# Performance work log

Hardware: AMD Instinct MI355X
Metric: run time of the kernel (lower is better)

Reference implementation:

```python
import jax, jax.numpy as jnp
import numpy as np

D_IN = 1024
D_MODEL = 1024
NUM_HEADS = 16
DEPTH = D_MODEL // NUM_HEADS


def setup_inputs() -> dict:
    key = jax.random.key(0)
    ks = jax.random.split(key, 7)
    B, N = 2, 2048
    s = 1.0 / np.sqrt(D_IN)
    return {
        "x": jax.random.normal(ks[0], (B, N, D_IN), dtype=jnp.float32),
        "Wq": jax.random.normal(ks[1], (D_IN, D_MODEL), dtype=jnp.float32) * s,
        "bq": jnp.zeros((D_MODEL,), dtype=jnp.float32),
        "Wk": jax.random.normal(ks[2], (D_IN, D_MODEL), dtype=jnp.float32) * s,
        "bk": jnp.zeros((D_MODEL,), dtype=jnp.float32),
        "Wv": jax.random.normal(ks[3], (D_IN, D_MODEL), dtype=jnp.float32) * s,
        "bv": jnp.zeros((D_MODEL,), dtype=jnp.float32),
    }


def _split_heads(t):
    B, N, _ = t.shape
    return t.reshape(B, N, NUM_HEADS, DEPTH).transpose(0, 2, 1, 3)  # [B,H,N,depth]


def reference(x, Wq, bq, Wk, bk, Wv, bv):
    B, N, _ = x.shape
    q = _split_heads(x @ Wq + bq)
    k = _split_heads(x @ Wk + bk)
    v = _split_heads(x @ Wv + bv)
    scale = 1.0 / jnp.sqrt(jnp.float32(DEPTH))
    attn = jnp.einsum("bhnd,bhmd->bhnm", q, k) * scale  # [B,H,N,N]
    attn = jax.nn.softmax(attn, axis=-1)
    out = jnp.einsum("bhnm,bhmd->bhnd", attn, v)
    return out.transpose(0, 2, 1, 3).reshape(B, N, D_MODEL)
```

## Files before the change

kernel.cpp:

```cpp
#include <hip/hip_runtime.h>
#include <cstdint>


#define SEQ_N 2048
#define NHEAD 16
#define DEPTH 64
#define SCALE_Q (0.125f * 1.44269504088896340736f)
#define M_OFF (-12.0f)

typedef short bf16x8 __attribute__((ext_vector_type(8)));
typedef short short4v __attribute__((ext_vector_type(4)));
typedef float f32x4 __attribute__((ext_vector_type(4)));

#define MFMA32(a, b, c) __builtin_amdgcn_mfma_f32_16x16x32_bf16((a), (b), (c), 0, 0, 0)

#if defined(__has_builtin)
#if __has_builtin(__builtin_amdgcn_exp2f)
#define FEXP2(x) __builtin_amdgcn_exp2f(x)
#endif
#endif
#ifndef FEXP2
#define FEXP2(x) exp2f(x)
#endif

__device__ __forceinline__ short f2b(float f) {
    union { float f; unsigned u; } v; v.f = f;
    unsigned u = v.u;
    return (short)((u + 0x7FFFu + ((u >> 16) & 1u)) >> 16);
}

__device__ __forceinline__ unsigned cvt_pk_bf16(float lo, float hi) {
    unsigned r;
    asm("v_cvt_pk_bf16_f32 %0, %1, %2" : "=v"(r) : "v"(lo), "v"(hi));
    return r;
}

__device__ __forceinline__ void gld_lds16(const void* g, void* l) {
    __builtin_amdgcn_global_load_lds(
        (const __attribute__((address_space(1))) unsigned int*)(uintptr_t)g,
        (__attribute__((address_space(3))) unsigned int*)(uintptr_t)l, 16, 0, 0);
}

__global__ __launch_bounds__(256) void cvt_all_kernel(
    const float* __restrict__ x, short* __restrict__ xb,
    const float* __restrict__ Wq, const float* __restrict__ Wk,
    const float* __restrict__ Wv, short* __restrict__ WT)
{
    __shared__ float tile[64][65];
    if (blockIdx.x < 2048) {
        const int i = blockIdx.x * 256 + threadIdx.x;
        const float4* xi = (const float4*)x + (size_t)i * 2;
        const float4 a = xi[0], c = xi[1];
        bf16x8 o;
        o[0] = f2b(a.x); o[1] = f2b(a.y); o[2] = f2b(a.z); o[3] = f2b(a.w);
        o[4] = f2b(c.x); o[5] = f2b(c.y); o[6] = f2b(c.z); o[7] = f2b(c.w);
        *((bf16x8*)xb + i) = o;
        return;
    }
    const int bid = blockIdx.x - 2048;
    const int mat = bid >> 8;
    const int t = bid & 255;
    const int k0 = (t >> 4) * 64, n0 = (t & 15) * 64;
    const float* W = (mat == 0) ? Wq : ((mat == 1) ? Wk : Wv);
    const int tt = threadIdx.x;
#pragma unroll
    for (int i = 0; i < 16; ++i) {
        const int idx = tt + i * 256;
        const int r = idx >> 6, c = idx & 63;
        tile[r][c] = W[(size_t)(k0 + r) * 1024 + n0 + c];
    }
    __syncthreads();
#pragma unroll
    for (int i = 0; i < 16; ++i) {
        const int idx = tt + i * 256;
        const int r = idx >> 6, c = idx & 63;
        WT[(size_t)(mat * 1024 + n0 + r) * 1024 + k0 + c] = f2b(tile[c][r]);
    }
}

__global__ __launch_bounds__(512, 2) void qkv_gemm_kernel(
    const short* __restrict__ A, const short* __restrict__ BT,
    const float* __restrict__ bq, const float* __restrict__ bk, const float* __restrict__ bv,
    short* __restrict__ Qb, short* __restrict__ Kb, short* __restrict__ VTb)
{
    __shared__ __align__(16) short sm[57344];
    const int tid = threadIdx.x;
    const int l = tid & 63, w = tid >> 6;
    const int lr = l & 15, lk = l >> 4;
    const int wr = w >> 2, wcn = w & 3;

    const int id2 = (blockIdx.x & 7) * 32 + (blockIdx.x >> 3);
    const int bm = id2 & 15, bn = id2 >> 4;
    const int row0 = bm * 256, col0 = bn * 192;

    const int gsrc8 = ((tid & 7) ^ ((tid >> 3) & 7)) << 3;
    const short* a_src = A + (size_t)(row0 + (tid >> 3)) * 1024 + gsrc8;
    const short* b_src = BT + (size_t)(col0 + (tid >> 3)) * 1024 + gsrc8;

    const int aBase = (wr * 128 + lr) * 64;
    const int bBase = (wcn * 48 + lr) * 64;
    const int asw0 = ((lk)     ^ (lr & 7)) << 3;
    const int asw1 = ((lk + 4) ^ (lr & 7)) << 3;

    f32x4 acc[8][3];
#pragma unroll
    for (int m = 0; m < 8; ++m)
#pragma unroll
        for (int n = 0; n < 3; ++n) acc[m][n] = (f32x4){0.f, 0.f, 0.f, 0.f};

#define GSTAGE(BUF, KT)                                                    \
    do {                                                                   \
        short* asb = sm + (BUF) * 16384;                                   \
        short* bsb = sm + 32768 + (BUF) * 12288;                           \
        gld_lds16(a_src + (KT) * 64,          &asb[tid * 8]);              \
        gld_lds16(a_src + (KT) * 64 + 65536,  &asb[tid * 8 + 4096]);       \
        gld_lds16(a_src + (KT) * 64 + 131072, &asb[tid * 8 + 8192]);       \
        gld_lds16(a_src + (KT) * 64 + 196608, &asb[tid * 8 + 12288]);      \
        gld_lds16(b_src + (KT) * 64,          &bsb[tid * 8]);              \
        gld_lds16(b_src + (KT) * 64 + 65536,  &bsb[tid * 8 + 4096]);       \
        gld_lds16(b_src + (KT) * 64 + 131072, &bsb[tid * 8 + 8192]);       \
    } while (0)

    GSTAGE(0, 0);

#pragma unroll 2
    for (int kt = 0; kt < 16; ++kt) {
        const int cur = kt & 1;
        if (kt + 1 < 16) {
            GSTAGE(cur ^ 1, kt + 1);
            asm volatile("s_waitcnt vmcnt(7)" ::: "memory");
        } else {
            asm volatile("s_waitcnt vmcnt(0)" ::: "memory");
        }
        __builtin_amdgcn_s_barrier();
        __builtin_amdgcn_sched_barrier(0);

        const short* Al = sm + cur * 16384;
        const short* Bl = sm + 32768 + cur * 12288;

        bf16x8 bfv[3][2];
#pragma unroll
        for (int n = 0; n < 3; ++n) {
            bfv[n][0] = *(const bf16x8*)(Bl + bBase + n * 1024 + asw0);
            bfv[n][1] = *(const bf16x8*)(Bl + bBase + n * 1024 + asw1);
        }
#pragma unroll
        for (int m = 0; m < 8; ++m) {
            bf16x8 a0 = *(const bf16x8*)(Al + aBase + m * 1024 + asw0);
            bf16x8 a1 = *(const bf16x8*)(Al + aBase + m * 1024 + asw1);
#pragma unroll
            for (int n = 0; n < 3; ++n) {
                acc[m][n] = MFMA32(a0, bfv[n][0], acc[m][n]);
                acc[m][n] = MFMA32(a1, bfv[n][1], acc[m][n]);
            }
        }

        __builtin_amdgcn_sched_barrier(0);
        __builtin_amdgcn_s_barrier();
    }
#undef GSTAGE

    short* Cl = sm;
#pragma unroll
    for (int n = 0; n < 3; ++n) {
        const int gb = col0 + wcn * 48 + n * 16;
        const int mat = gb >> 10;
        const int jj = (gb + lr) & 1023;
        if (mat < 2) {
            const float bias = ((mat == 0) ? bq : bk)[jj];
            const float sc = (mat == 0) ? SCALE_Q : 1.0f;
            const int cc = wcn * 48 + n * 16 + lr;
#pragma unroll
            for (int m = 0; m < 8; ++m) {
                const int rbase = wr * 128 + m * 16 + lk * 4;
#pragma unroll
                for (int r = 0; r < 4; ++r)
                    Cl[(rbase + r) * 200 + cc] = f2b((acc[m][n][r] + bias) * sc);
            }
        } else {
            const float bias = bv[jj];
            const int h = jj >> 6, d = jj & 63;
#pragma unroll
            for (int m = 0; m < 8; ++m) {
                const int grow0 = row0 + wr * 128 + m * 16 + lk * 4;
                const int bb = grow0 >> 11, ns0 = grow0 & 2047;
                const int g = (ns0 >> 2) & 15;
                const int gp = (g & 8) | ((g & 3) << 1) | ((g >> 2) & 1);
                const int nsp = (ns0 & ~63) | (gp << 2);
                short4v pv;
#pragma unroll
                for (int r = 0; r < 4; ++r) pv[r] = f2b(acc[m][n][r] + bias);
                *(short4v*)(VTb + ((size_t)(bb * NHEAD + h) * DEPTH + d) * SEQ_N + nsp) = pv;
            }
        }
    }
    __syncthreads();
    {
        const int row = tid >> 1, half = tid & 1;
        const int grow = row0 + row;
        const int bb = grow >> 11, ns = grow & 2047;
#pragma unroll
        for (int i = 0; i < 12; ++i) {
            const int cc = half * 96 + i * 8;
            const int gc = col0 + cc;
            const int mat = gc >> 10;
            if (mat < 2) {
                short* O = mat ? Kb : Qb;
                const int h = (gc & 1023) >> 6, d0 = gc & 63;
                *(bf16x8*)(O + ((size_t)(bb * NHEAD + h) * SEQ_N + ns) * DEPTH + d0) =
                    *(const bf16x8*)(Cl + row * 200 + cc);
            }
        }
    }
}


__device__ __forceinline__ float exppack32_lane(const f32x4 s[4], bf16x8 pb[2]) {
    float rs = 0.f;
#pragma unroll
    for (int kk = 0; kk < 2; ++kk) {
        union { unsigned u[4]; bf16x8 v; } pk;
#pragma unroll
        for (int hh = 0; hh < 2; ++hh) {
            const int c = 2 * kk + hh;
            const float p0 = FEXP2(s[c][0]);
            const float p1 = FEXP2(s[c][1]);
            const float p2 = FEXP2(s[c][2]);
            const float p3 = FEXP2(s[c][3]);
            rs += (p0 + p1) + (p2 + p3);
            pk.u[2 * hh]     = cvt_pk_bf16(p0, p1);
            pk.u[2 * hh + 1] = cvt_pk_bf16(p2, p3);
        }
        pb[kk] = pk.v;
    }
    return rs;
}

#define NT 16

__global__ __launch_bounds__(256, 2) void attn_kernel(
    const short* __restrict__ Qb, const short* __restrict__ Kb,
    const short* __restrict__ VTb, float* __restrict__ out)
{
    __shared__ short smem[2][16384];

    const int tid = threadIdx.x;
    const int l = tid & 63, w = tid >> 6;
    const int lr = l & 15, lk = l >> 4;

    const int hb = blockIdx.x;
    const int slot = hb >> 3;
    const int bh = (hb & 7) * 4 + (slot >> 4);
    const int qt = slot & 15;
    const int b = bh >> 4, h = bh & 15;

    const int qw = qt * 128 + w * 32;

    const short* Qg = Qb + ((size_t)bh * SEQ_N + qw + lr) * DEPTH + lk * 8;
    const bf16x8 bq00 = *(const bf16x8*)(Qg);
    const bf16x8 bq01 = *(const bf16x8*)(Qg + 32);
    const bf16x8 bq10 = *(const bf16x8*)(Qg + 16 * DEPTH);
    const bf16x8 bq11 = *(const bf16x8*)(Qg + 16 * DEPTH + 32);

    const short* Kg = Kb + (size_t)bh * SEQ_N * DEPTH;
    const short* Vg = VTb + (size_t)bh * DEPTH * SEQ_N;

    const int srow = tid >> 3;
    const int sg = (tid & 7) ^ (srow & 7);
    const short* Ksrc = Kg + (size_t)srow * DEPTH + sg * 8;
    const short* Vsrc = Vg + (size_t)srow * SEQ_N + sg * 8;

#define STAGE(BUF, T)                                                            \
    do {                                                                         \
        const int key0_ = (T) * 128;                                             \
        short* dst = &smem[BUF][w * 512];                                        \
        gld_lds16(Ksrc + (size_t)key0_ * DEPTH, dst);                            \
        gld_lds16(Ksrc + (size_t)(key0_ + 32) * DEPTH, dst + 2048);              \
        gld_lds16(Ksrc + (size_t)(key0_ + 64) * DEPTH, dst + 4096);              \
        gld_lds16(Ksrc + (size_t)(key0_ + 96) * DEPTH, dst + 6144);              \
        gld_lds16(Vsrc + key0_, dst + 8192);                                     \
        gld_lds16(Vsrc + key0_ + 32 * SEQ_N, dst + 10240);                       \
        gld_lds16(Vsrc + key0_ + 64, dst + 12288);                               \
        gld_lds16(Vsrc + key0_ + 64 + 32 * SEQ_N, dst + 14336);                  \
    } while (0)

    const short* s0p = &smem[0][0];
    const int aoff0 = lr * 64 + (((lk    ) ^ (lr & 7)) << 3);
    const int aoff1 = lr * 64 + (((lk + 4) ^ (lr & 7)) << 3);

    f32x4 acc0[4], acc1[4];
#pragma unroll
    for (int n = 0; n < 4; ++n) {
        acc0[n] = (f32x4){0.f, 0.f, 0.f, 0.f};
        acc1[n] = (f32x4){0.f, 0.f, 0.f, 0.f};
    }
    float l0 = 0.f, l1 = 0.f;

    STAGE(0, 0);
    asm volatile("s_waitcnt vmcnt(0)" ::: "memory");
    __builtin_amdgcn_s_barrier();
    __builtin_amdgcn_sched_barrier(0);

#pragma unroll 2
    for (int t = 0; t < NT; ++t) {
        const int cur = t & 1;
        const int tn = (t + 1 < NT) ? (t + 1) : (NT - 1);
        STAGE(cur ^ 1, tn);

#pragma unroll
        for (int ss = 0; ss < 2; ++ss) {
            const int sub = ss ^ (w & 1);
            const short* Kl = s0p + cur * 16384 + sub * 4096;
            const short* Vl = Kl + 8192;

            bf16x8 kf[4][2], vf[4][2];
#pragma unroll
            for (int c = 0; c < 4; ++c) {
                kf[c][0] = *(const bf16x8*)(Kl + c * 1024 + aoff0);
                kf[c][1] = *(const bf16x8*)(Kl + c * 1024 + aoff1);
            }
#pragma unroll
            for (int n = 0; n < 4; ++n) {
                vf[n][0] = *(const bf16x8*)(Vl + n * 1024 + aoff0);
                vf[n][1] = *(const bf16x8*)(Vl + n * 1024 + aoff1);
            }

            f32x4 s0[4], s1[4];
            __builtin_amdgcn_s_setprio(1);
#pragma unroll
            for (int c = 0; c < 4; ++c) {
                f32x4 a = (f32x4){M_OFF, M_OFF, M_OFF, M_OFF};
                a = MFMA32(kf[c][0], bq00, a);
                a = MFMA32(kf[c][1], bq01, a);
                s0[c] = a;
                f32x4 bb2 = (f32x4){M_OFF, M_OFF, M_OFF, M_OFF};
                bb2 = MFMA32(kf[c][0], bq10, bb2);
                bb2 = MFMA32(kf[c][1], bq11, bb2);
                s1[c] = bb2;
            }
            __builtin_amdgcn_s_setprio(0);

            bf16x8 pb0[2], pb1[2];
            l0 += exppack32_lane(s0, pb0);
            l1 += exppack32_lane(s1, pb1);

            __builtin_amdgcn_s_setprio(1);
#pragma unroll
            for (int n = 0; n < 4; ++n) {
                acc0[n] = MFMA32(vf[n][0], pb0[0], acc0[n]);
                acc0[n] = MFMA32(vf[n][1], pb0[1], acc0[n]);
                acc1[n] = MFMA32(vf[n][0], pb1[0], acc1[n]);
                acc1[n] = MFMA32(vf[n][1], pb1[1], acc1[n]);
            }
            __builtin_amdgcn_s_setprio(0);
        }

        asm volatile("s_waitcnt vmcnt(0)" ::: "memory");
        __builtin_amdgcn_s_barrier();
        __builtin_amdgcn_sched_barrier(0);
    }
#undef STAGE

    l0 += __shfl_xor(l0, 16); l0 += __shfl_xor(l0, 32);
    l1 += __shfl_xor(l1, 16); l1 += __shfl_xor(l1, 32);

    const float inv0 = 1.0f / l0, inv1 = 1.0f / l1;
    float* o0 = out + ((size_t)b * SEQ_N + qw + lr) * 1024 + h * 64 + lk * 4;
    float* o1 = o0 + (size_t)16 * 1024;
#pragma unroll
    for (int n = 0; n < 4; ++n) {
        const f32x4 v0 = acc0[n] * inv0;
        const f32x4 v1 = acc1[n] * inv1;
        *(f32x4*)(o0 + n * 16) = v0;
        *(f32x4*)(o1 + n * 16) = v1;
    }
}

extern "C" void kernel_launch(void* const* d_in, const int* in_sizes, int n_in,
                              void* d_out, int out_size, void* d_ws, size_t ws_size,
                              hipStream_t stream) {
    const float* x  = (const float*)d_in[0];
    const float* Wq = (const float*)d_in[1];
    const float* bq = (const float*)d_in[2];
    const float* Wk = (const float*)d_in[3];
    const float* bk = (const float*)d_in[4];
    const float* Wv = (const float*)d_in[5];
    const float* bv = (const float*)d_in[6];
    float* out = (float*)d_out;

    char* ws = (char*)d_ws;
    short* xb  = (short*)(ws);
    short* WT  = (short*)(ws + (8  << 20));
    short* Qb  = (short*)(ws + (14 << 20));
    short* Kb  = (short*)(ws + (22 << 20));
    short* VTb = (short*)(ws + (30 << 20));

    cvt_all_kernel<<<2816, 256, 0, stream>>>(x, xb, Wq, Wk, Wv, WT);
    qkv_gemm_kernel<<<256, 512, 0, stream>>>(xb, WT, bq, bk, bv, Qb, Kb, VTb);
    attn_kernel<<<512, 256, 0, stream>>>(Qb, Kb, VTb, out);
}
```

Measured before the change: 83.72 us.

## Fuse x fp32-to-bf16 conversion into QKV GEMM A-tile loading

Drops the separate x conversion pass. The GEMM now loads fp32 x tiles into registers, converts them with packed bf16 conversion, and writes them to LDS after the MFMA compute of each k-step, while the B tiles still go directly from global to LDS. This removes one write and one read of the bf16 copy of x through global memory. The cost is more registers (launch bounds drop to 1 block per CU), twice the A-side global bytes per tile, and conversion and LDS-store work inside the GEMM loop.

```diff
diff --git a/kernel.cpp b/kernel.cpp
--- a/kernel.cpp
+++ b/kernel.cpp
@@ -41,23 +41,12 @@
         (__attribute__((address_space(3))) unsigned int*)(uintptr_t)l, 16, 0, 0);
 }
 
-__global__ __launch_bounds__(256) void cvt_all_kernel(
-    const float* __restrict__ x, short* __restrict__ xb,
+__global__ __launch_bounds__(256) void cvt_w_kernel(
     const float* __restrict__ Wq, const float* __restrict__ Wk,
     const float* __restrict__ Wv, short* __restrict__ WT)
 {
     __shared__ float tile[64][65];
-    if (blockIdx.x < 2048) {
-        const int i = blockIdx.x * 256 + threadIdx.x;
-        const float4* xi = (const float4*)x + (size_t)i * 2;
-        const float4 a = xi[0], c = xi[1];
-        bf16x8 o;
-        o[0] = f2b(a.x); o[1] = f2b(a.y); o[2] = f2b(a.z); o[3] = f2b(a.w);
-        o[4] = f2b(c.x); o[5] = f2b(c.y); o[6] = f2b(c.z); o[7] = f2b(c.w);
-        *((bf16x8*)xb + i) = o;
-        return;
-    }
-    const int bid = blockIdx.x - 2048;
+    const int bid = blockIdx.x;
     const int mat = bid >> 8;
     const int t = bid & 255;
     const int k0 = (t >> 4) * 64, n0 = (t & 15) * 64;
@@ -78,8 +67,8 @@
     }
 }
 
-__global__ __launch_bounds__(512, 2) void qkv_gemm_kernel(
-    const short* __restrict__ A, const short* __restrict__ BT,
+__global__ __launch_bounds__(512, 1) void qkv_gemm_kernel(
+    const float* __restrict__ X, const short* __restrict__ BT,
     const float* __restrict__ bq, const float* __restrict__ bk, const float* __restrict__ bv,
     short* __restrict__ Qb, short* __restrict__ Kb, short* __restrict__ VTb)
 {
@@ -94,7 +83,7 @@
     const int row0 = bm * 256, col0 = bn * 192;
 
     const int gsrc8 = ((tid & 7) ^ ((tid >> 3) & 7)) << 3;
-    const short* a_src = A + (size_t)(row0 + (tid >> 3)) * 1024 + gsrc8;
+    const float* x_src = X + (size_t)(row0 + (tid >> 3)) * 1024 + gsrc8;
     const short* b_src = BT + (size_t)(col0 + (tid >> 3)) * 1024 + gsrc8;
 
     const int aBase = (wr * 128 + lr) * 64;
@@ -108,29 +97,53 @@
 #pragma unroll
         for (int n = 0; n < 3; ++n) acc[m][n] = (f32x4){0.f, 0.f, 0.f, 0.f};
 
-#define GSTAGE(BUF, KT)                                                    \
-    do {                                                                   \
-        short* asb = sm + (BUF) * 16384;                                   \
-        short* bsb = sm + 32768 + (BUF) * 12288;                           \
-        gld_lds16(a_src + (KT) * 64,          &asb[tid * 8]);              \
-        gld_lds16(a_src + (KT) * 64 + 65536,  &asb[tid * 8 + 4096]);       \
-        gld_lds16(a_src + (KT) * 64 + 131072, &asb[tid * 8 + 8192]);       \
-        gld_lds16(a_src + (KT) * 64 + 196608, &asb[tid * 8 + 12288]);      \
-        gld_lds16(b_src + (KT) * 64,          &bsb[tid * 8]);              \
-        gld_lds16(b_src + (KT) * 64 + 65536,  &bsb[tid * 8 + 4096]);       \
-        gld_lds16(b_src + (KT) * 64 + 131072, &bsb[tid * 8 + 8192]);       \
+    float4 la[4][2];
+
+#define ALOAD(K1)                                                              \
+    do {                                                                       \
+        _Pragma("unroll")                                                      \
+        for (int j = 0; j < 4; ++j) {                                          \
+            la[j][0] = *(const float4*)(x_src + j * 65536 + (K1));             \
+            la[j][1] = *(const float4*)(x_src + j * 65536 + (K1) + 4);         \
+        }                                                                      \
     } while (0)
 
-    GSTAGE(0, 0);
+#define BSTAGE(BUF, KT)                                                        \
+    do {                                                                       \
+        short* bsb = sm + 32768 + (BUF) * 12288;                               \
+        gld_lds16(b_src + (KT) * 64,          &bsb[tid * 8]);                  \
+        gld_lds16(b_src + (KT) * 64 + 65536,  &bsb[tid * 8 + 4096]);           \
+        gld_lds16(b_src + (KT) * 64 + 131072, &bsb[tid * 8 + 8192]);           \
+    } while (0)
+
+#define AWRITE(BUF)                                                            \
+    do {                                                                       \
+        short* asb = sm + (BUF) * 16384;                                       \
+        _Pragma("unroll")                                                      \
+        for (int j = 0; j < 4; ++j) {                                          \
+            union { unsigned u[4]; bf16x8 v; } pk;                             \
+            pk.u[0] = cvt_pk_bf16(la[j][0].x, la[j][0].y);                     \
+            pk.u[1] = cvt_pk_bf16(la[j][0].z, la[j][0].w);                     \
+            pk.u[2] = cvt_pk_bf16(la[j][1].x, la[j][1].y);                     \
+            pk.u[3] = cvt_pk_bf16(la[j][1].z, la[j][1].w);                     \
+            *(bf16x8*)(asb + tid * 8 + j * 4096) = pk.v;                       \
+        }                                                                      \
+    } while (0)
+
+    ALOAD(0);
+    BSTAGE(0, 0);
+    asm volatile("s_waitcnt vmcnt(3)" ::: "memory");
+    AWRITE(0);
 
 #pragma unroll 2
     for (int kt = 0; kt < 16; ++kt) {
         const int cur = kt & 1;
         if (kt + 1 < 16) {
-            GSTAGE(cur ^ 1, kt + 1);
-            asm volatile("s_waitcnt vmcnt(7)" ::: "memory");
+            ALOAD((kt + 1) * 64);
+            BSTAGE(cur ^ 1, kt + 1);
+            asm volatile("s_waitcnt vmcnt(11) lgkmcnt(0)" ::: "memory");
         } else {
-            asm volatile("s_waitcnt vmcnt(0)" ::: "memory");
+            asm volatile("s_waitcnt vmcnt(0) lgkmcnt(0)" ::: "memory");
         }
         __builtin_amdgcn_s_barrier();
         __builtin_amdgcn_sched_barrier(0);
@@ -155,10 +168,16 @@
             }
         }
 
+        if (kt + 1 < 16) {
+            asm volatile("s_waitcnt vmcnt(3)" ::: "memory");
+            AWRITE(cur ^ 1);
+        }
         __builtin_amdgcn_sched_barrier(0);
         __builtin_amdgcn_s_barrier();
     }
-#undef GSTAGE
+#undef ALOAD
+#undef BSTAGE
+#undef AWRITE
 
     short* Cl = sm;
 #pragma unroll
@@ -389,13 +408,12 @@
     float* out = (float*)d_out;
 
     char* ws = (char*)d_ws;
-    short* xb  = (short*)(ws);
-    short* WT  = (short*)(ws + (8  << 20));
-    short* Qb  = (short*)(ws + (14 << 20));
-    short* Kb  = (short*)(ws + (22 << 20));
-    short* VTb = (short*)(ws + (30 << 20));
-
-    cvt_all_kernel<<<2816, 256, 0, stream>>>(x, xb, Wq, Wk, Wv, WT);
-    qkv_gemm_kernel<<<256, 512, 0, stream>>>(xb, WT, bq, bk, bv, Qb, Kb, VTb);
+    short* WT  = (short*)(ws);
+    short* Qb  = (short*)(ws + (6  << 20));
+    short* Kb  = (short*)(ws + (14 << 20));
+    short* VTb = (short*)(ws + (22 << 20));
+
+    cvt_w_kernel<<<768, 256, 0, stream>>>(Wq, Wk, Wv, WT);
+    qkv_gemm_kernel<<<256, 512, 0, stream>>>(x, WT, bq, bk, bv, Qb, Kb, VTb);
     attn_kernel<<<512, 256, 0, stream>>>(Qb, Kb, VTb, out);
 }
```

Result: slower. 89.38 us (+6.7%).
